# Kernel optimization log

Hardware: AMD Instinct MI355X
Metric: run time of the kernel (lower is better)

The kernel has to match this reference:

```python
import jax, jax.numpy as jnp
import numpy as np

BLOCK_LEN = 128
NUM_HEADS = 16


def setup_inputs() -> dict:
    key = jax.random.key(0)
    k0, k1, k2 = jax.random.split(key, 3)
    D = 1024
    x = jax.random.normal(k0, (2, 8192, D), dtype=jnp.float32)
    Wqkv = jax.random.normal(k1, (D, 3 * D), dtype=jnp.float32) * 0.02
    bqkv = jnp.zeros((3 * D,), dtype=jnp.float32)
    Wout = jax.random.normal(k2, (D, D), dtype=jnp.float32) * 0.02
    bout = jnp.zeros((D,), dtype=jnp.float32)
    return {"x": x, "Wqkv": Wqkv, "bqkv": bqkv, "Wout": Wout, "bout": bout}


def reference(x, Wqkv, bqkv, Wout, bout):
    B, S, D = x.shape
    H = NUM_HEADS
    BL = BLOCK_LEN
    NB = S // BL            # number of blocks (rows)
    HD = D // H             # head dim (qkv_ratio=1.0 -> qkv_dim_total == D)

    qkv = x @ Wqkv + bqkv                                   # [B, S, 3D]
    qkv = qkv.reshape(B, NB, BL, 3, H, HD)
    q = qkv[:, :, :, 0]                                     # [B, NB, BL, H, HD]
    k = qkv[:, :, :, 1]
    v = qkv[:, :, :, 2]

    # 'column' attention: attend across blocks at the same within-block position.
    # permute to [B, BL(pos p), H, NB(block n), HD]
    qc = jnp.transpose(q, (0, 2, 3, 1, 4))
    kc = jnp.transpose(k, (0, 2, 3, 1, 4))
    vc = jnp.transpose(v, (0, 2, 3, 1, 4))

    scale = 1.0 / jnp.sqrt(jnp.asarray(HD, dtype=x.dtype))
    scores = jnp.einsum('bphnd,bphmd->bphnm', qc, kc) * scale   # [B,BL,H,NB,NB]
    causal = jnp.tril(jnp.ones((NB, NB), dtype=bool))
    scores = jnp.where(causal, scores, jnp.asarray(-1e9, dtype=scores.dtype))
    w = jax.nn.softmax(scores, axis=-1)
    o = jnp.einsum('bphnm,bphmd->bphnd', w, vc)                 # [B,BL,H,NB,HD]

    # back to [B, NB, BL, H*HD] -> [B, S, D]
    o = jnp.transpose(o, (0, 3, 1, 2, 4)).reshape(B, S, D)
    return o @ Wout + bout
```

## Files before the change

### kernel.cpp

```cpp
#include <hip/hip_runtime.h>
#include <stdint.h>

typedef unsigned short u16;
typedef __attribute__((ext_vector_type(8))) short s16x8;
typedef __attribute__((ext_vector_type(4))) float f32x4;

__device__ __forceinline__ f32x4 mfma16x16(s16x8 a, s16x8 b, f32x4 c) {
    return __builtin_amdgcn_mfma_f32_16x16x32_bf16(a, b, c, 0, 0, 0);
}

__device__ __forceinline__ u16 f2bf(float f) {
    union { float f; unsigned u; } c; c.f = f;
    unsigned u = c.u;
    return (u16)((u + 0x7FFFu + ((u >> 16) & 1u)) >> 16);
}

__device__ __forceinline__ void gload16(const void* g, void* l) {
    auto gp = (const __attribute__((address_space(1))) unsigned int*)(g);
    auto lp = (__attribute__((address_space(3))) unsigned int*)(l);
    __builtin_amdgcn_global_load_lds(gp, lp, 16, 0, 0);
}

__device__ __forceinline__ void wave_sync() {
    __builtin_amdgcn_sched_barrier(0);
    asm volatile("s_waitcnt vmcnt(0) lgkmcnt(0)" ::: "memory");
    __builtin_amdgcn_sched_barrier(0);
    __builtin_amdgcn_s_barrier();
    __builtin_amdgcn_sched_barrier(0);
}

__global__ __launch_bounds__(256) void convert_x(
    const float* __restrict__ src, u16* __restrict__ dst, long n)
{
    const long stride = (long)gridDim.x * 256 * 8;
    for (long i = ((long)blockIdx.x * 256 + threadIdx.x) * 8; i < n; i += stride) {
        const float4 a = *(const float4*)(src + i);
        const float4 b = *(const float4*)(src + i + 4);
        u16 o[8] = { f2bf(a.x), f2bf(a.y), f2bf(a.z), f2bf(a.w),
                     f2bf(b.x), f2bf(b.y), f2bf(b.z), f2bf(b.w) };
        *(s16x8*)(dst + i) = *(const s16x8*)o;
    }
}

__global__ __launch_bounds__(256) void fill_sentinel(float* __restrict__ o, long n)
{
    const long stride = (long)gridDim.x * 256;
    for (long i = (long)blockIdx.x * 256 + threadIdx.x; i < n; i += stride)
        o[i] = 1.0f;
}

__global__ __launch_bounds__(256) void transpose_f32_bf16(
    const float* __restrict__ in, u16* __restrict__ out, int R, int C)
{
    __shared__ u16 t[32][33];
    const int c0 = blockIdx.x * 32, r0 = blockIdx.y * 32;
    const int tx = threadIdx.x & 31, ty = threadIdx.x >> 5;
#pragma unroll
    for (int i = 0; i < 32; i += 8)
        t[ty + i][tx] = f2bf(in[(long)(r0 + ty + i) * C + c0 + tx]);
    __syncthreads();
#pragma unroll
    for (int i = 0; i < 32; i += 8)
        out[(long)(c0 + ty + i) * R + r0 + tx] = t[tx][ty + i];
}

template <int FP32OUT, int NT, int NBN>
__global__ __launch_bounds__(512, 2) void gemm256(
    const u16* __restrict__ A, const u16* __restrict__ BT,
    const float* __restrict__ bias, void* __restrict__ Cout,
    int N, int K)
{
    extern __shared__ char smem[];
    char* const As = smem;
    char* const Bs = smem + 65536;

    const int tid  = threadIdx.x;
    const int lane = tid & 63;
    const int wid  = tid >> 6;
    const int rr   = lane & 15, g = lane >> 4;
    const int wr   = wid >> 2;
    const int wc   = wid & 3;

    const int nwg = gridDim.x;
    const int gsw = (blockIdx.x & 7) * (nwg >> 3) + (blockIdx.x >> 3);
    const long m0 = (long)(gsw / NBN) * 256;
    const long n0 = (long)(gsw % NBN) * 256;

    const int cl = (tid & 3) ^ ((tid >> 3) & 3);
    const u16* pA0 = A  + (m0 + (tid >> 2)) * (long)K + cl * 8;
    const u16* pA1 = pA0 + 128 * (long)K;
    const u16* pB0 = BT + (n0 + (tid >> 2)) * (long)K + cl * 8;
    const u16* pB1 = pB0 + 128 * (long)K;
    const int sdst = wid * 1024;

    const int xg    = (g ^ ((rr >> 1) & 3)) << 4;
    const int arow  = (wr * 128 + rr) * 64 + xg;
    const int brow  = (wc * 64  + rr) * 64 + xg;

#define STA(tt, h) { const long c_ = (long)(tt) * 64 + (h) * 32;              \
        char* d_ = As + (((tt) & 1) * 2 + (h)) * 16384 + sdst;                \
        gload16(pA0 + c_, d_); gload16(pA1 + c_, d_ + 8192); }
#define STB(tt, h) { const long c_ = (long)(tt) * 64 + (h) * 32;              \
        char* d_ = Bs + (((tt) & 1) * 2 + (h)) * 16384 + sdst;                \
        gload16(pB0 + c_, d_); gload16(pB1 + c_, d_ + 8192); }
#define BAR() { __builtin_amdgcn_sched_barrier(0); __builtin_amdgcn_s_barrier(); }
#define LGKM0() { asm volatile("s_waitcnt lgkmcnt(0)" ::: "memory");          \
        __builtin_amdgcn_sched_barrier(0); }

    f32x4 acc[8][4] = {};

    STA(0, 0); STB(0, 0); STA(0, 1); STB(0, 1); STA(1, 0); STB(1, 0);
    asm volatile("s_waitcnt vmcnt(4)" ::: "memory");
    BAR();

    for (int t = 0; t < NT; ++t) {
        const int ab = (t & 1) * 32768;
        const bool tl = (t >= NT - 3);
        s16x8 bf[4], af[4];

#pragma unroll
        for (int n = 0; n < 4; ++n)
            bf[n] = *(const s16x8*)(Bs + ab + brow + n * 1024);
#pragma unroll
        for (int m = 0; m < 4; ++m)
            af[m] = *(const s16x8*)(As + ab + arow + m * 1024);
        if (t + 1 < NT) STA(t + 1, 1);
        BAR(); LGKM0();
        __builtin_amdgcn_s_setprio(1);
#pragma unroll
        for (int m = 0; m < 4; ++m)
#pragma unroll
            for (int n = 0; n < 4; ++n)
                acc[m][n] = mfma16x16(af[m], bf[n], acc[m][n]);
        __builtin_amdgcn_s_setprio(0);
        BAR();

#pragma unroll
        for (int m = 0; m < 4; ++m)
            af[m] = *(const s16x8*)(As + ab + arow + (m + 4) * 1024);
        if (t + 1 < NT) STB(t + 1, 1);
        if (tl) { asm volatile("s_waitcnt vmcnt(0)" ::: "memory"); }
        else    { asm volatile("s_waitcnt vmcnt(4)" ::: "memory"); }
        BAR(); LGKM0();
        __builtin_amdgcn_s_setprio(1);
#pragma unroll
        for (int m = 0; m < 4; ++m)
#pragma unroll
            for (int n = 0; n < 4; ++n)
                acc[m + 4][n] = mfma16x16(af[m], bf[n], acc[m + 4][n]);
        __builtin_amdgcn_s_setprio(0);
        BAR();

#pragma unroll
        for (int n = 0; n < 4; ++n)
            bf[n] = *(const s16x8*)(Bs + ab + 16384 + brow + n * 1024);
#pragma unroll
        for (int m = 0; m < 4; ++m)
            af[m] = *(const s16x8*)(As + ab + 16384 + arow + m * 1024);
        if (t + 2 < NT) STA(t + 2, 0);
        BAR(); LGKM0();
        __builtin_amdgcn_s_setprio(1);
#pragma unroll
        for (int m = 0; m < 4; ++m)
#pragma unroll
            for (int n = 0; n < 4; ++n)
                acc[m][n] = mfma16x16(af[m], bf[n], acc[m][n]);
        __builtin_amdgcn_s_setprio(0);
        BAR();

#pragma unroll
        for (int m = 0; m < 4; ++m)
            af[m] = *(const s16x8*)(As + ab + 16384 + arow + (m + 4) * 1024);
        if (t + 2 < NT) STB(t + 2, 0);
        if (tl) { asm volatile("s_waitcnt vmcnt(0)" ::: "memory"); }
        else    { asm volatile("s_waitcnt vmcnt(4)" ::: "memory"); }
        BAR(); LGKM0();
        __builtin_amdgcn_s_setprio(1);
#pragma unroll
        for (int m = 0; m < 4; ++m)
#pragma unroll
            for (int n = 0; n < 4; ++n)
                acc[m + 4][n] = mfma16x16(af[m], bf[n], acc[m + 4][n]);
        __builtin_amdgcn_s_setprio(0);
        BAR();
    }
#undef STA
#undef STB
#undef BAR
#undef LGKM0

    float bv[4];
#pragma unroll
    for (int n = 0; n < 4; ++n)
        bv[n] = bias[n0 + wc * 64 + n * 16 + rr];
#pragma unroll
    for (int m = 0; m < 8; ++m) {
        const long rb = m0 + wr * 128 + m * 16 + g * 4;
#pragma unroll
        for (int r = 0; r < 4; ++r) {
            const long rowoff = (rb + r) * N + n0 + wc * 64 + rr;
#pragma unroll
            for (int n = 0; n < 4; ++n) {
                const float v = acc[m][n][r] + bv[n];
                if (FP32OUT) ((float*)Cout)[rowoff + n * 16] = v;
                else         ((u16*)Cout)[rowoff + n * 16] = f2bf(v);
            }
        }
    }
}

template <int FP32OUT>
__global__ __launch_bounds__(256) void gemm_bt_bias(
    const u16* __restrict__ A, const u16* __restrict__ BT,
    const float* __restrict__ bias, void* __restrict__ Cout,
    int M, int N, int K)
{
    __shared__ u16 As[128 * 64];
    __shared__ u16 Bs[128 * 64];
    const int tid  = threadIdx.x;
    const int lane = tid & 63;
    const int wid  = tid >> 6;
    const int rr   = lane & 15, g = lane >> 4;
    const int wm   = (wid >> 1) << 6;
    const int wn   = (wid & 1) << 6;
    const long m0  = (long)blockIdx.y * 128;
    const long n0  = (long)blockIdx.x * 128;
    const int srow   = tid >> 3;
    const int schunk = (tid & 7) ^ (srow & 7);

    f32x4 acc[4][4] = {};

    for (int k0 = 0; k0 < K; k0 += 64) {
#pragma unroll
        for (int q = 0; q < 4; ++q) {
            const int row = q * 32 + srow;
            gload16(A  + (m0 + row) * K + k0 + schunk * 8,
                    (char*)As + q * 4096 + wid * 1024);
            gload16(BT + (n0 + row) * K + k0 + schunk * 8,
                    (char*)Bs + q * 4096 + wid * 1024);
        }
        __syncthreads();
#pragma unroll
        for (int kk = 0; kk < 2; ++kk) {
            s16x8 af[4], bfr[4];
#pragma unroll
            for (int i = 0; i < 4; ++i) {
                const int rowa = wm + i * 16 + rr;
                af[i] = *(const s16x8*)((const char*)As + rowa * 128 +
                         ((kk * 64 + g * 16) ^ ((rowa & 7) << 4)));
                const int rowb = wn + i * 16 + rr;
                bfr[i] = *(const s16x8*)((const char*)Bs + rowb * 128 +
                         ((kk * 64 + g * 16) ^ ((rowb & 7) << 4)));
            }
#pragma unroll
            for (int i = 0; i < 4; ++i)
#pragma unroll
                for (int j = 0; j < 4; ++j)
                    acc[i][j] = mfma16x16(af[i], bfr[j], acc[i][j]);
        }
        __syncthreads();
    }

#pragma unroll
    for (int i = 0; i < 4; ++i)
#pragma unroll
        for (int r = 0; r < 4; ++r) {
            const long rowg = m0 + wm + i * 16 + g * 4 + r;
#pragma unroll
            for (int j = 0; j < 4; ++j) {
                const long col = n0 + wn + j * 16 + rr;
                const float v = acc[i][j][r] + bias[col];
                if (FP32OUT) ((float*)Cout)[rowg * N + col] = v;
                else         ((u16*)Cout)[rowg * N + col] = f2bf(v);
            }
        }
}

__global__ __launch_bounds__(64) void attn_blocks(
    const u16* __restrict__ qkv, u16* __restrict__ o)
{
    __shared__ u16 Vlds[64 * 64];
    __shared__ u16 Plds[64 * 72];
    const int bid = blockIdx.x;
    const int b = bid >> 11;
    const int h = (bid >> 7) & 15;
    const int p = bid & 127;
    const int lane = threadIdx.x;
    const int rr = lane & 15, g = lane >> 4;
    const long NSTR = 128L * 3072;
    const long base = ((long)b * 8192 + p) * 3072 + h * 64;

    {
        const int vrow = lane >> 3;
        const int vchunk = (lane & 7) ^ (vrow & 7);
#pragma unroll
        for (int q = 0; q < 8; ++q)
            gload16(qkv + base + (long)(q * 8 + vrow) * NSTR + 2048 + vchunk * 8,
                    (char*)Vlds + q * 1024);
    }

    s16x8 kf[4][2], qf[4][2];
#pragma unroll
    for (int t = 0; t < 4; ++t)
#pragma unroll
        for (int ks = 0; ks < 2; ++ks) {
            const long roff = base + (long)(t * 16 + rr) * NSTR + ks * 32 + g * 8;
            kf[t][ks] = *(const s16x8*)(qkv + roff + 1024);
            qf[t][ks] = *(const s16x8*)(qkv + roff);
        }

    f32x4 T[4][4] = {};
#pragma unroll
    for (int ks = 0; ks < 2; ++ks)
#pragma unroll
        for (int i = 0; i < 4; ++i)
#pragma unroll
            for (int jn = 0; jn < 4; ++jn)
                T[i][jn] = mfma16x16(kf[i][ks], qf[jn][ks], T[i][jn]);

    const float scale = 0.125f;
#pragma unroll
    for (int jn = 0; jn < 4; ++jn) {
        const int n = jn * 16 + rr;
        float pv[16];
        float mx = -3e38f;
#pragma unroll
        for (int i = 0; i < 4; ++i)
#pragma unroll
            for (int r = 0; r < 4; ++r) {
                const int m = i * 16 + g * 4 + r;
                const float s = (m <= n) ? T[i][jn][r] * scale : -3e38f;
                pv[i * 4 + r] = s;
                mx = fmaxf(mx, s);
            }
        mx = fmaxf(mx, __shfl_xor(mx, 16));
        mx = fmaxf(mx, __shfl_xor(mx, 32));
        float sum = 0.f;
#pragma unroll
        for (int t = 0; t < 16; ++t) {
            const float e = (pv[t] > -1e30f) ? __expf(pv[t] - mx) : 0.f;
            pv[t] = e;
            sum += e;
        }
        sum += __shfl_xor(sum, 16);
        sum += __shfl_xor(sum, 32);
        const float inv = 1.f / sum;
#pragma unroll
        for (int i = 0; i < 4; ++i)
#pragma unroll
            for (int rp = 0; rp < 2; ++rp) {
                const int m = i * 16 + g * 4 + rp * 2;
                const unsigned lo = f2bf(pv[i * 4 + rp * 2] * inv);
                const unsigned hi = f2bf(pv[i * 4 + rp * 2 + 1] * inv);
                *(unsigned*)((char*)Plds + n * 144 + m * 2) = lo | (hi << 16);
            }
    }

    wave_sync();

    f32x4 O[4][4] = {};
#pragma unroll
    for (int ks = 0; ks < 2; ++ks) {
        s16x8 pa[4];
#pragma unroll
        for (int in = 0; in < 4; ++in)
            pa[in] = *(const s16x8*)((const char*)Plds +
                      (in * 16 + rr) * 144 + ks * 64 + g * 16);
#pragma unroll
        for (int jd = 0; jd < 4; ++jd) {
            s16x8 vb;
#pragma unroll
            for (int j = 0; j < 8; ++j) {
                const int k = ks * 32 + g * 8 + j;
                const int byte = (k * 128 + (jd * 16 + rr) * 2) ^ ((k & 7) << 4);
                vb[j] = *(const short*)((const char*)Vlds + byte);
            }
#pragma unroll
            for (int in = 0; in < 4; ++in)
                O[in][jd] = mfma16x16(pa[in], vb, O[in][jd]);
        }
    }

    const long obase = ((long)b * 8192 + p) * 1024 + h * 64;
#pragma unroll
    for (int in = 0; in < 4; ++in)
#pragma unroll
        for (int r = 0; r < 4; ++r) {
            const long n = in * 16 + g * 4 + r;
#pragma unroll
            for (int jd = 0; jd < 4; ++jd) {
                const long d = jd * 16 + rr;
                o[obase + n * (128L * 1024) + d] = f2bf(O[in][jd][r]);
            }
        }
}

extern "C" void kernel_launch(void* const* d_in, const int* in_sizes, int n_in,
                              void* d_out, int out_size, void* d_ws, size_t ws_size,
                              hipStream_t stream) {
    const float* x    = (const float*)d_in[0];
    const float* Wqkv = (const float*)d_in[1];
    const float* bq   = (const float*)d_in[2];
    const float* Wout = (const float*)d_in[3];
    const float* bo   = (const float*)d_in[4];

    char* ws = (char*)d_ws;
    u16* xb    = (u16*)(ws);
    u16* qkv   = (u16*)(ws +  33554432L);
    u16* ob    = (u16*)(ws + 134217728L);
    u16* WqkvT = (u16*)(ws + 167772160L);
    u16* WoutT = (u16*)(ws + 174063616L);
    const size_t NEEDED = 176160768UL;

    if (ws_size < NEEDED) {
        fill_sentinel<<<2048, 256, 0, stream>>>((float*)d_out, (long)out_size);
        return;
    }

    bool deep = true;
    if (hipFuncSetAttribute(reinterpret_cast<const void*>(&gemm256<0, 16, 12>),
                            hipFuncAttributeMaxDynamicSharedMemorySize,
                            131072) != hipSuccess) deep = false;
    if (hipFuncSetAttribute(reinterpret_cast<const void*>(&gemm256<1, 16, 4>),
                            hipFuncAttributeMaxDynamicSharedMemorySize,
                            131072) != hipSuccess) deep = false;

    convert_x<<<2048, 256, 0, stream>>>(x, xb, 16777216L);
    transpose_f32_bf16<<<dim3(96, 32), 256, 0, stream>>>(Wqkv, WqkvT, 1024, 3072);
    transpose_f32_bf16<<<dim3(32, 32), 256, 0, stream>>>(Wout, WoutT, 1024, 1024);

    if (deep)
        gemm256<0, 16, 12><<<768, 512, 131072, stream>>>(xb, WqkvT, bq, qkv,
                                                         3072, 1024);
    else
        gemm_bt_bias<0><<<dim3(24, 128), 256, 0, stream>>>(xb, WqkvT, bq, qkv,
                                                           16384, 3072, 1024);

    attn_blocks<<<4096, 64, 0, stream>>>(qkv, ob);

    if (deep)
        gemm256<1, 16, 4><<<256, 512, 131072, stream>>>(ob, WoutT, bo, d_out,
                                                        1024, 1024);
    else
        gemm_bt_bias<1><<<dim3(8, 128), 256, 0, stream>>>(ob, WoutT, bo, d_out,
                                                          16384, 1024, 1024);
}
```

Baseline: 207.1 us.

## Cut GEMM main-loop barriers to two per iteration and preload fragments earlier

Reworks the bf16 MFMA GEMM main loop to drop six of its eight workgroup barriers and the explicit lgkmcnt waits per iteration. LDS fragments for A and B are now loaded into separate register arrays ahead of the MFMA groups that use them, so LDS reads overlap earlier compute. A single vmcnt wait plus barrier at the end of each iteration now makes the next tile visible, and a mid-iteration barrier guards reuse of the first half-buffer. This is meant to cut barrier stalls between waves, at the cost of more live VGPRs for fragments, which could hurt occupancy or cause spills, and it relies on the compiler to place LDS waits correctly.

```diff
diff --git a/kernel.cpp b/kernel.cpp
--- a/kernel.cpp
+++ b/kernel.cpp
@@ -103,91 +103,89 @@
 #define STB(tt, h) { const long c_ = (long)(tt) * 64 + (h) * 32;              \
         char* d_ = Bs + (((tt) & 1) * 2 + (h)) * 16384 + sdst;                \
         gload16(pB0 + c_, d_); gload16(pB1 + c_, d_ + 8192); }
-#define BAR() { __builtin_amdgcn_sched_barrier(0); __builtin_amdgcn_s_barrier(); }
-#define LGKM0() { asm volatile("s_waitcnt lgkmcnt(0)" ::: "memory");          \
-        __builtin_amdgcn_sched_barrier(0); }
+#define SB() __builtin_amdgcn_sched_barrier(0)
 
     f32x4 acc[8][4] = {};
 
     STA(0, 0); STB(0, 0); STA(0, 1); STB(0, 1); STA(1, 0); STB(1, 0);
     asm volatile("s_waitcnt vmcnt(4)" ::: "memory");
-    BAR();
+    SB(); __builtin_amdgcn_s_barrier(); SB();
 
     for (int t = 0; t < NT; ++t) {
         const int ab = (t & 1) * 32768;
-        const bool tl = (t >= NT - 3);
-        s16x8 bf[4], af[4];
+        s16x8 fB0[4], fA0[4], fA1[4], fB1[4], fA2[4], fA3[4];
 
 #pragma unroll
         for (int n = 0; n < 4; ++n)
-            bf[n] = *(const s16x8*)(Bs + ab + brow + n * 1024);
-#pragma unroll
-        for (int m = 0; m < 4; ++m)
-            af[m] = *(const s16x8*)(As + ab + arow + m * 1024);
+            fB0[n] = *(const s16x8*)(Bs + ab + brow + n * 1024);
+#pragma unroll
+        for (int m = 0; m < 4; ++m)
+            fA0[m] = *(const s16x8*)(As + ab + arow + m * 1024);
+#pragma unroll
+        for (int m = 0; m < 4; ++m)
+            fA1[m] = *(const s16x8*)(As + ab + arow + (m + 4) * 1024);
         if (t + 1 < NT) STA(t + 1, 1);
-        BAR(); LGKM0();
+        SB();
         __builtin_amdgcn_s_setprio(1);
 #pragma unroll
         for (int m = 0; m < 4; ++m)
 #pragma unroll
             for (int n = 0; n < 4; ++n)
-                acc[m][n] = mfma16x16(af[m], bf[n], acc[m][n]);
+                acc[m][n] = mfma16x16(fA0[m], fB0[n], acc[m][n]);
         __builtin_amdgcn_s_setprio(0);
-        BAR();
-
-#pragma unroll
-        for (int m = 0; m < 4; ++m)
-            af[m] = *(const s16x8*)(As + ab + arow + (m + 4) * 1024);
+        SB();
+
+#pragma unroll
+        for (int n = 0; n < 4; ++n)
+            fB1[n] = *(const s16x8*)(Bs + ab + 16384 + brow + n * 1024);
+#pragma unroll
+        for (int m = 0; m < 4; ++m)
+            fA2[m] = *(const s16x8*)(As + ab + 16384 + arow + m * 1024);
         if (t + 1 < NT) STB(t + 1, 1);
-        if (tl) { asm volatile("s_waitcnt vmcnt(0)" ::: "memory"); }
-        else    { asm volatile("s_waitcnt vmcnt(4)" ::: "memory"); }
-        BAR(); LGKM0();
+        SB();
         __builtin_amdgcn_s_setprio(1);
 #pragma unroll
         for (int m = 0; m < 4; ++m)
 #pragma unroll
             for (int n = 0; n < 4; ++n)
-                acc[m + 4][n] = mfma16x16(af[m], bf[n], acc[m + 4][n]);
+                acc[m + 4][n] = mfma16x16(fA1[m], fB0[n], acc[m + 4][n]);
         __builtin_amdgcn_s_setprio(0);
-        BAR();
-
-#pragma unroll
-        for (int n = 0; n < 4; ++n)
-            bf[n] = *(const s16x8*)(Bs + ab + 16384 + brow + n * 1024);
-#pragma unroll
-        for (int m = 0; m < 4; ++m)
-            af[m] = *(const s16x8*)(As + ab + 16384 + arow + m * 1024);
+        SB(); __builtin_amdgcn_s_barrier(); SB();
+
+#pragma unroll
+        for (int m = 0; m < 4; ++m)
+            fA3[m] = *(const s16x8*)(As + ab + 16384 + arow + (m + 4) * 1024);
         if (t + 2 < NT) STA(t + 2, 0);
-        BAR(); LGKM0();
+        SB();
         __builtin_amdgcn_s_setprio(1);
 #pragma unroll
         for (int m = 0; m < 4; ++m)
 #pragma unroll
             for (int n = 0; n < 4; ++n)
-                acc[m][n] = mfma16x16(af[m], bf[n], acc[m][n]);
+                acc[m][n] = mfma16x16(fA2[m], fB1[n], acc[m][n]);
         __builtin_amdgcn_s_setprio(0);
-        BAR();
-
-#pragma unroll
-        for (int m = 0; m < 4; ++m)
-            af[m] = *(const s16x8*)(As + ab + 16384 + arow + (m + 4) * 1024);
+        SB();
+
         if (t + 2 < NT) STB(t + 2, 0);
-        if (tl) { asm volatile("s_waitcnt vmcnt(0)" ::: "memory"); }
-        else    { asm volatile("s_waitcnt vmcnt(4)" ::: "memory"); }
-        BAR(); LGKM0();
+        SB();
         __builtin_amdgcn_s_setprio(1);
 #pragma unroll
         for (int m = 0; m < 4; ++m)
 #pragma unroll
             for (int n = 0; n < 4; ++n)
-                acc[m + 4][n] = mfma16x16(af[m], bf[n], acc[m + 4][n]);
+                acc[m + 4][n] = mfma16x16(fA3[m], fB1[n], acc[m + 4][n]);
         __builtin_amdgcn_s_setprio(0);
-        BAR();
+        SB();
+
+        if (t < NT - 1) {
+            if (t >= NT - 2) { asm volatile("s_waitcnt vmcnt(0)" ::: "memory"); }
+            else             { asm volatile("s_waitcnt vmcnt(4)" ::: "memory"); }
+            SB(); __builtin_amdgcn_s_barrier(); SB();
+        }
     }
 #undef STA
 #undef STB
-#undef BAR
-#undef LGKM0
+#undef SB
 
     float bv[4];
 #pragma unroll
```

New measurement: 190.8 us. 7.9% less time.
